# Kernel optimization log

Hardware: AMD Instinct MI355X
Metric: run time of the kernel (lower is better)

Reference implementation:

```python
import jax, jax.numpy as jnp
import numpy as np

EPS = 1e-6
NEG = 1e9

def _norm(x):
    # Normalizator math with alpha=1, gamma=0 (torch.std is unbiased -> ddof=1)
    m = jnp.mean(x, axis=-1, keepdims=True)
    s = jnp.std(x, axis=-1, ddof=1, keepdims=True)
    return (x - m) / (s + EPS)

def setup_inputs() -> dict:
    key = jax.random.key(0)
    ks = jax.random.split(key, 16)
    T, S, D, F, L = 4096, 4096, 512, 2048, 4
    sc = 1.0 / np.sqrt(D)
    scf = 1.0 / np.sqrt(F)
    return {
        "current_tgt_output": jax.random.normal(ks[0], (T, D), jnp.float32),
        "encoder_output": jax.random.normal(ks[1], (S, D), jnp.float32),
        "cross_mask": jax.random.randint(ks[2], (T, S), 0, 2).astype(jnp.float32),
        "Wq": jax.random.normal(ks[3], (L, D, D), jnp.float32) * sc,
        "Wk": jax.random.normal(ks[4], (L, D, D), jnp.float32) * sc,
        "Wv": jax.random.normal(ks[5], (L, D, D), jnp.float32) * sc,
        "Wo": jax.random.normal(ks[6], (L, D, D), jnp.float32) * sc,
        "Cq": jax.random.normal(ks[7], (L, D, D), jnp.float32) * sc,
        "Ck": jax.random.normal(ks[8], (L, D, D), jnp.float32) * sc,
        "Cv": jax.random.normal(ks[9], (L, D, D), jnp.float32) * sc,
        "Co": jax.random.normal(ks[10], (L, D, D), jnp.float32) * sc,
        "W1": jax.random.normal(ks[11], (L, D, F), jnp.float32) * sc,
        "W2": jax.random.normal(ks[12], (L, F, D), jnp.float32) * scf,
        "alpha": jnp.ones((1,), jnp.float32),
        "gamma": jnp.zeros((1,), jnp.float32),
        "input_ids": jax.random.randint(ks[13], (T,), 0, S),
        "training_step": T,
        "training_mode": 1,
    }

def reference(current_tgt_output, encoder_output, cross_mask, Wq, Wk, Wv, Wo,
              Cq, Ck, Cv, Co, W1, W2, alpha, gamma, input_ids,
              training_step, training_mode):
    T = training_step
    x = current_tgt_output[:T] if training_mode else current_tgt_output
    cm = cross_mask[:T]                                  # [T, S]
    # the python double-loop -> single vectorized gather: self_mask[i,k]=cross_mask[i, input_ids[k]]
    self_mask = cm[:, input_ids]                         # [T, T]
    sbias = (self_mask - 1.0) * NEG                      # additive mask bias
    cbias = (cm - 1.0) * NEG
    D = x.shape[-1]
    scale = 1.0 / jnp.sqrt(jnp.asarray(D, x.dtype))
    L = Wq.shape[0]
    for l in range(L):
        h = _norm(x)
        q, k, v = h @ Wq[l], h @ Wk[l], h @ Wv[l]
        a = jax.nn.softmax(q @ k.T * scale + sbias, axis=-1)
        x = x + (a @ v) @ Wo[l]
        h = _norm(x)
        q = h @ Cq[l]
        k, v = encoder_output @ Ck[l], encoder_output @ Cv[l]
        a = jax.nn.softmax(q @ k.T * scale + cbias, axis=-1)
        x = x + (a @ v) @ Co[l]
        h = _norm(x)
        x = x + jax.nn.relu(h @ W1[l]) @ W2[l]
    return alpha * _norm(x) + gamma
```

## Files before the change

### kernel.cpp

```cpp
#include <hip/hip_runtime.h>
#include <math.h>

typedef _Float16 half_t;
typedef unsigned int u32;
typedef unsigned short u16;
typedef float f32x4 __attribute__((ext_vector_type(4)));
typedef _Float16 f16x8 __attribute__((ext_vector_type(8)));
typedef _Float16 f16x4 __attribute__((ext_vector_type(4)));

#define T_DIM 4096
#define S_DIM 4096
#define D_DIM 512
#define F_DIM 2048
#define NLAYER 4
#define KVS ((size_t)4096 * 512)

__device__ __forceinline__ void gload16(const void* g, void* l) {
    __builtin_amdgcn_global_load_lds(
        (const __attribute__((address_space(1))) u32*)g,
        (__attribute__((address_space(3))) u32*)l, 16, 0, 0);
}

template<int N> __device__ __forceinline__ void wait_vm() {
    if constexpr (N == 0) asm volatile("s_waitcnt vmcnt(0)" ::: "memory");
    else if constexpr (N == 3) asm volatile("s_waitcnt vmcnt(3)" ::: "memory");
    else if constexpr (N == 4) asm volatile("s_waitcnt vmcnt(4)" ::: "memory");
    else if constexpr (N == 6) asm volatile("s_waitcnt vmcnt(6)" ::: "memory");
    else if constexpr (N == 8) asm volatile("s_waitcnt vmcnt(8)" ::: "memory");
}
__device__ __forceinline__ void wait_lgkm0() {
    asm volatile("s_waitcnt lgkmcnt(0)" ::: "memory");
}

template<int BN, int EPI>
__global__ __launch_bounds__(512)
void gemm_nt(const half_t* __restrict__ A, int lda,
             const half_t* __restrict__ B, int ldb,
             int N, int K, int gx,
             half_t* __restrict__ D1, half_t* __restrict__ D2,
             half_t* __restrict__ D3, int ldd)
{
    constexpr int BM = 128, BK = 64;
    constexpr int NF = BN / 32;
    constexpr int LPT = 2 + BN / 64;
    constexpr int NSLOT = (BN == 64) ? 3 : 2;
    __shared__ half_t As[NSLOT][BM * BK];
    __shared__ half_t Bs[NSLOT][BN * BK];

    const int tid  = threadIdx.x;
    const int wave = tid >> 6;
    const int lane = tid & 63;

    const int nb  = gridDim.x;
    const int bid = blockIdx.x;
    const int nid = (bid & 7) * (nb >> 3) + (bid >> 3);
    const int bx  = nid % gx;
    const int by  = nid / gx;
    const int bm = by * BM, bn = bx * BN;

    const int wm = (wave >> 1) * 32;
    const int wn = (wave & 1) * (BN / 2);
    const int kq = lane >> 4;
    const int rr = lane & 15;
    const int scol = (((lane & 7) ^ (lane >> 3)) << 3);

    f32x4 acc[2][NF];
#pragma unroll
    for (int m = 0; m < 2; ++m)
#pragma unroll
        for (int n = 0; n < NF; ++n)
            acc[m][n] = f32x4{0.f, 0.f, 0.f, 0.f};

    auto stage = [&](int buf, int k0) {
#pragma unroll
        for (int c = 0; c < 2; ++c) {
            const int row = wave * 16 + c * 8 + (lane >> 3);
            gload16(A + (size_t)(bm + row) * lda + k0 + scol,
                    (char*)&As[buf][0] + (wave * 2 + c) * 1024 + lane * 16);
        }
        if constexpr (BN == 64) {
            const int row = wave * 8 + (lane >> 3);
            gload16(B + (size_t)(bn + row) * ldb + k0 + scol,
                    (char*)&Bs[buf][0] + wave * 1024 + lane * 16);
        } else {
#pragma unroll
            for (int c = 0; c < 2; ++c) {
                const int row = wave * 16 + c * 8 + (lane >> 3);
                gload16(B + (size_t)(bn + row) * ldb + k0 + scol,
                        (char*)&Bs[buf][0] + (wave * 2 + c) * 1024 + lane * 16);
            }
        }
    };

    const int nt = K / BK;
    stage(0, 0);
    if constexpr (NSLOT == 3) stage(1, BK);
    int cur = 0, pf = NSLOT - 1;
    for (int t = 0; t < nt; ++t) {
        if (t + 1 < nt) wait_vm<(NSLOT - 2) * LPT>(); else wait_vm<0>();
        __builtin_amdgcn_s_barrier();
        if (t + NSLOT - 1 < nt) stage(pf, (t + NSLOT - 1) * BK);
#pragma unroll
        for (int ks = 0; ks < 2; ++ks) {
            f16x8 af[2], bf[NF];
#pragma unroll
            for (int m = 0; m < 2; ++m) {
                const int r = wm + m * 16 + rr;
                af[m] = *(const f16x8*)&As[cur][r * BK + (((ks * 4 + kq) ^ (r & 7)) << 3)];
            }
#pragma unroll
            for (int n = 0; n < NF; ++n) {
                const int r = wn + n * 16 + rr;
                bf[n] = *(const f16x8*)&Bs[cur][r * BK + (((ks * 4 + kq) ^ (r & 7)) << 3)];
            }
#pragma unroll
            for (int m = 0; m < 2; ++m)
#pragma unroll
                for (int n = 0; n < NF; ++n)
                    acc[m][n] = __builtin_amdgcn_mfma_f32_16x16x32_f16(af[m], bf[n], acc[m][n], 0, 0, 0);
        }
        cur = (cur + 1 == NSLOT) ? 0 : cur + 1;
        pf  = (pf  + 1 == NSLOT) ? 0 : pf  + 1;
    }

    const int r0 = bm + wm + (lane >> 4) * 4;
#pragma unroll
    for (int m = 0; m < 2; ++m)
#pragma unroll
        for (int n = 0; n < NF; ++n) {
            const int c = bn + wn + n * 16 + rr;
            if (EPI == 2) {
#pragma unroll
                for (int i = 0; i < 4; ++i)
                    D1[(size_t)(r0 + m * 16 + i) * ldd + c] = (half_t)acc[m][n][i];
            } else if (EPI == 5) {
                half_t* Dst = (bn < 512) ? D1 : (bn < 1024) ? D2 : D3;
                const int sub = c & 511;
#pragma unroll
                for (int i = 0; i < 4; ++i)
                    Dst[(size_t)(r0 + m * 16 + i) * 512 + sub] = (half_t)acc[m][n][i];
            } else {
                const int l = c >> 10;
                const int sub = c & 1023;
                half_t* Dst = (sub < 512) ? (D2 + l * KVS) : (D3 + l * KVS);
                const int d = sub & 511;
#pragma unroll
                for (int i = 0; i < 4; ++i)
                    Dst[(size_t)(r0 + m * 16 + i) * 512 + d] = (half_t)acc[m][n][i];
            }
        }
}

__global__ __launch_bounds__(512)
void gemm_fold(const half_t* __restrict__ Wt, const half_t* __restrict__ V,
               half_t* __restrict__ Out, int zSA, long zSB, long zSD)
{
    constexpr int BM = 128, BK = 64, BN = 64, NSLOT = 3, LPT = 3;
    __shared__ half_t As[NSLOT][BM * BK];
    __shared__ half_t Bs[NSLOT][BN * BK];

    const half_t* A = Wt + (size_t)blockIdx.z * zSA;
    const half_t* B = V  + (size_t)blockIdx.z * zSB;
    half_t* D = Out + (size_t)blockIdx.z * zSD;

    const int tid  = threadIdx.x;
    const int wave = tid >> 6;
    const int lane = tid & 63;

    const int nb  = gridDim.x;
    const int bid = blockIdx.x;
    const int nid = (bid & 7) * (nb >> 3) + (bid >> 3);
    const int bx = nid & 63, by = nid >> 6;
    const int bm = by * BM, bn = bx * BN;

    const int wm = (wave >> 1) * 32;
    const int wn = (wave & 1) * 32;
    const int kq = lane >> 4;
    const int rr = lane & 15;
    const int scol = (((lane & 7) ^ (lane >> 3)) << 3);

    f32x4 acc[2][2];
#pragma unroll
    for (int m = 0; m < 2; ++m)
#pragma unroll
        for (int n = 0; n < 2; ++n)
            acc[m][n] = f32x4{0.f, 0.f, 0.f, 0.f};

    auto stage = [&](int buf, int k0) {
#pragma unroll
        for (int c = 0; c < 2; ++c) {
            const int row = wave * 16 + c * 8 + (lane >> 3);
            gload16(A + (size_t)(bm + row) * 512 + k0 + scol,
                    (char*)&As[buf][0] + (wave * 2 + c) * 1024 + lane * 16);
        }
        const int row = wave * 8 + (lane >> 3);
        gload16(B + (size_t)(bn + row) * 512 + k0 + scol,
                (char*)&Bs[buf][0] + wave * 1024 + lane * 16);
    };

    const int nt = 512 / BK;
    stage(0, 0);
    stage(1, BK);
    int cur = 0, pf = 2;
    for (int t = 0; t < nt; ++t) {
        if (t + 1 < nt) wait_vm<LPT>(); else wait_vm<0>();
        __builtin_amdgcn_s_barrier();
        if (t + 2 < nt) stage(pf, (t + 2) * BK);
#pragma unroll
        for (int ks = 0; ks < 2; ++ks) {
            f16x8 af[2], bf[2];
#pragma unroll
            for (int m = 0; m < 2; ++m) {
                const int r = wm + m * 16 + rr;
                af[m] = *(const f16x8*)&As[cur][r * BK + (((ks * 4 + kq) ^ (r & 7)) << 3)];
            }
#pragma unroll
            for (int n = 0; n < 2; ++n) {
                const int r = wn + n * 16 + rr;
                bf[n] = *(const f16x8*)&Bs[cur][r * BK + (((ks * 4 + kq) ^ (r & 7)) << 3)];
            }
#pragma unroll
            for (int m = 0; m < 2; ++m)
#pragma unroll
                for (int n = 0; n < 2; ++n)
                    acc[m][n] = __builtin_amdgcn_mfma_f32_16x16x32_f16(af[m], bf[n], acc[m][n], 0, 0, 0);
        }
        cur = (cur + 1 == NSLOT) ? 0 : cur + 1;
        pf  = (pf  + 1 == NSLOT) ? 0 : pf  + 1;
    }

    const int r0 = bm + wm + (lane >> 4) * 4;
#pragma unroll
    for (int m = 0; m < 2; ++m)
#pragma unroll
        for (int n = 0; n < 2; ++n) {
            const int c = bn + wn + n * 16 + rr;
#pragma unroll
            for (int i = 0; i < 4; ++i)
                D[(size_t)(r0 + m * 16 + i) * 4096 + c] = (half_t)acc[m][n][i];
        }
}

template<int EPI, int SPLITK = 1, int P16 = 1>
__global__ __launch_bounds__(256)
void gemm97(const half_t* __restrict__ A, int lda,
            const half_t* __restrict__ B, int ldb,
            int K, int gx, half_t* __restrict__ D,
            float* __restrict__ Fout, int ldd)
{
    constexpr int BK = 32, NSLOT = 3, LPT = 4;
    __shared__ half_t As[NSLOT][128 * BK];
    __shared__ half_t Bs[NSLOT][128 * BK];

    const int tid  = threadIdx.x;
    const int wave = tid >> 6;
    const int lane = tid & 63;

    const int nb  = gridDim.x;
    const int bid = blockIdx.x;
    const int nid = (bid & 7) * (nb >> 3) + (bid >> 3);
    const int gy  = nb / (gx * SPLITK);
    const int bx  = nid % gx;
    const int tmp = nid / gx;
    const int by  = tmp % gy;
    const int kz  = tmp / gy;
    const int bm = by * 128, bn = bx * 128;

    const int Keff = K / SPLITK;
    A += (size_t)kz * Keff;
    B += (size_t)kz * Keff;

    const int wm = (wave >> 1) * 64;
    const int wn = (wave & 1) * 64;
    const int kq = lane >> 4;
    const int rr = lane & 15;
    const int srow = lane >> 2;
    const int scol = (((lane & 3) ^ ((lane >> 3) & 3)) << 3);
    const int kqa  = kq ^ ((rr >> 1) & 3);

    const half_t* Abase = A + (size_t)(bm + wave * 16 + srow) * lda + scol;
    const half_t* Bbase = B + (size_t)(bn + wave * 16 + srow) * ldb + scol;

    f32x4 acc[4][4];
#pragma unroll
    for (int m = 0; m < 4; ++m)
#pragma unroll
        for (int n = 0; n < 4; ++n)
            acc[m][n] = f32x4{0.f, 0.f, 0.f, 0.f};

    auto stage = [&](int buf, int k0) {
#pragma unroll
        for (int c = 0; c < 2; ++c)
            gload16(Abase + (size_t)c * 64 * lda + k0,
                    (char*)&As[buf][0] + c * 4096 + wave * 1024 + lane * 16);
#pragma unroll
        for (int c = 0; c < 2; ++c)
            gload16(Bbase + (size_t)c * 64 * ldb + k0,
                    (char*)&Bs[buf][0] + c * 4096 + wave * 1024 + lane * 16);
    };

    const int nt = Keff / BK;
    stage(0, 0);
    stage(1, BK);
    int cur = 0, pf = 2;
    for (int t = 0; t < nt; ++t) {
        if (t + 1 < nt) wait_vm<LPT>(); else wait_vm<0>();
        __builtin_amdgcn_s_barrier();
        if (t + 2 < nt) stage(pf, (t + 2) * BK);
        f16x8 af[4], bf[4];
#pragma unroll
        for (int m = 0; m < 4; ++m)
            af[m] = *(const f16x8*)&As[cur][(wm + m * 16 + rr) * BK + kqa * 8];
#pragma unroll
        for (int n = 0; n < 4; ++n)
            bf[n] = *(const f16x8*)&Bs[cur][(wn + n * 16 + rr) * BK + kqa * 8];
#pragma unroll
        for (int m = 0; m < 4; ++m)
#pragma unroll
            for (int n = 0; n < 4; ++n)
                acc[m][n] = __builtin_amdgcn_mfma_f32_16x16x32_f16(af[m], bf[n], acc[m][n], 0, 0, 0);
        cur = (cur == 2) ? 0 : cur + 1;
        pf  = (pf  == 2) ? 0 : pf + 1;
    }

    const int r0 = bm + wm + (lane >> 4) * 4;
    const int soff = kz * gx * 128;
#pragma unroll
    for (int m = 0; m < 4; ++m)
#pragma unroll
        for (int n = 0; n < 4; ++n) {
            const int c = bn + wn + n * 16 + rr;
#pragma unroll
            for (int i = 0; i < 4; ++i) {
                float v = acc[m][n][i];
                const size_t r = r0 + m * 16 + i;
                if constexpr (SPLITK > 1) {
                    if constexpr (P16) D[r * ldd + soff + c] = (half_t)v;
                    else               Fout[r * ldd + soff + c] = v;
                } else {
                    if (EPI == 4) v = fmaxf(v, 0.f);
                    D[r * ldd + c] = (half_t)v;
                }
            }
        }
}

__global__ __launch_bounds__(256, 4)
void gemm_logits(const half_t* __restrict__ A, const half_t* __restrict__ B,
                 const u32* __restrict__ bits, half_t* __restrict__ D)
{
    constexpr int BK = 32, NSLOT = 3, LPT = 4, nt = 16;
    __shared__ half_t As[NSLOT][128 * BK];
    __shared__ half_t Bs[NSLOT][128 * BK];

    const int tid  = threadIdx.x;
    const int wave = tid >> 6;
    const int lane = tid & 63;

    const int nb  = gridDim.x;
    const int bid = blockIdx.x;
    const int nid = (bid & 7) * (nb >> 3) + (bid >> 3);
    const int bx = nid & 31, by = nid >> 5;
    const int bm = by * 128, bn = bx * 128;

    const int wm = (wave >> 1) * 64;
    const int wn = (wave & 1) * 64;
    const int kq = lane >> 4;
    const int rr = lane & 15;
    const int srow = lane >> 2;
    const int scol = (((lane & 3) ^ ((lane >> 3) & 3)) << 3);
    const int kqa  = kq ^ ((rr >> 1) & 3);

    const half_t* Abase = A + (size_t)(bm + wave * 16 + srow) * 512 + scol;
    const half_t* Bbase = B + (size_t)(bn + wave * 16 + srow) * 512 + scol;

    f32x4 acc[4][4];
#pragma unroll
    for (int m = 0; m < 4; ++m)
#pragma unroll
        for (int n = 0; n < 4; ++n)
            acc[m][n] = f32x4{0.f, 0.f, 0.f, 0.f};

    auto stage = [&](int buf, int k0) {
#pragma unroll
        for (int c = 0; c < 2; ++c)
            gload16(Abase + (size_t)c * 64 * 512 + k0,
                    (char*)&As[buf][0] + c * 4096 + wave * 1024 + lane * 16);
#pragma unroll
        for (int c = 0; c < 2; ++c)
            gload16(Bbase + (size_t)c * 64 * 512 + k0,
                    (char*)&Bs[buf][0] + c * 4096 + wave * 1024 + lane * 16);
    };

    stage(0, 0);
    stage(1, BK);
    int cur = 0, pf = 2;
    for (int t = 0; t < nt; ++t) {
        if (t + 1 < nt) wait_vm<LPT>(); else wait_vm<0>();
        __builtin_amdgcn_s_barrier();
        if (t + 2 < nt) stage(pf, (t + 2) * BK);
        f16x8 af[4], bf[4];
#pragma unroll
        for (int m = 0; m < 4; ++m)
            af[m] = *(const f16x8*)&As[cur][(wm + m * 16 + rr) * BK + kqa * 8];
#pragma unroll
        for (int n = 0; n < 4; ++n)
            bf[n] = *(const f16x8*)&Bs[cur][(wn + n * 16 + rr) * BK + kqa * 8];
#pragma unroll
        for (int m = 0; m < 4; ++m)
#pragma unroll
            for (int n = 0; n < 4; ++n)
                acc[m][n] = __builtin_amdgcn_mfma_f32_16x16x32_f16(af[m], bf[n], acc[m][n], 0, 0, 0);
        cur = (cur == 2) ? 0 : cur + 1;
        pf  = (pf  == 2) ? 0 : pf + 1;
    }

    const int g4 = (lane >> 4) * 4;
    const int r0 = bm + wm + g4;
    const int wordbase = (bn + wn) >> 5;
#pragma unroll
    for (int m = 0; m < 4; ++m)
#pragma unroll
        for (int i = 0; i < 4; ++i) {
            const int r = r0 + m * 16 + i;
            const u32 w01 = bits[(size_t)r * 128 + wordbase];
            const u32 w23 = bits[(size_t)r * 128 + wordbase + 1];
            acc[m][0][i] += (((w01 >> rr) & 1u) ? 0.f : -1e9f);
            acc[m][1][i] += (((w01 >> (16 + rr)) & 1u) ? 0.f : -1e9f);
            acc[m][2][i] += (((w23 >> rr) & 1u) ? 0.f : -1e9f);
            acc[m][3][i] += (((w23 >> (16 + rr)) & 1u) ? 0.f : -1e9f);
        }
#pragma unroll
    for (int m = 0; m < 4; ++m)
#pragma unroll
        for (int n = 0; n < 4; ++n) {
            const int c = bn + wn + n * 16 + rr;
#pragma unroll
            for (int i = 0; i < 4; ++i)
                D[(size_t)(r0 + m * 16 + i) * 4096 + c] = (half_t)acc[m][n][i];
        }
}

__global__ __launch_bounds__(256)
void row_stats(const half_t* __restrict__ logits, float2* __restrict__ rowstat)
{
    const int t = blockIdx.x;
    const half_t* row = logits + (size_t)t * S_DIM;
    __shared__ float red[8];
    const int tid = threadIdx.x, wave = tid >> 6, lane = tid & 63;
    const int s0 = tid * 16;
    f16x8 h0 = *(const f16x8*)&row[s0];
    f16x8 h1 = *(const f16x8*)&row[s0 + 8];
    float z[16];
    float lmax = -3.0e38f;
#pragma unroll
    for (int q = 0; q < 16; ++q) {
        z[q] = (float)((q < 8) ? h0[q & 7] : h1[q & 7]);
        lmax = fmaxf(lmax, z[q]);
    }
#pragma unroll
    for (int off = 32; off; off >>= 1) lmax = fmaxf(lmax, __shfl_xor(lmax, off));
    if (lane == 0) red[wave] = lmax;
    __syncthreads();
    const float mx = fmaxf(fmaxf(red[0], red[1]), fmaxf(red[2], red[3]));
    float lsum = 0.f;
#pragma unroll
    for (int q = 0; q < 16; ++q) lsum += __expf(z[q] - mx);
#pragma unroll
    for (int off = 32; off; off >>= 1) lsum += __shfl_xor(lsum, off);
    if (lane == 0) red[4 + wave] = lsum;
    __syncthreads();
    if (tid == 0)
        rowstat[t] = float2{mx, 1.f / (red[4] + red[5] + red[6] + red[7])};
}

__global__ __launch_bounds__(256)
void gemm_pv(const half_t* __restrict__ A, const half_t* __restrict__ B,
             const float2* __restrict__ rowstat, half_t* __restrict__ D)
{
    constexpr int BK = 32, NSLOT = 3, Keff = 1024, nt = 32;
    __shared__ half_t As[NSLOT][128 * BK];
    __shared__ half_t Bs[NSLOT][128 * BK];

    const int tid = threadIdx.x, wave = tid >> 6, lane = tid & 63;
    const int nb = gridDim.x, bid = blockIdx.x;
    const int nid = (bid & 7) * (nb >> 3) + (bid >> 3);
    const int bx = nid & 3;
    const int tmp = nid >> 2;
    const int by = tmp & 31, kz = tmp >> 5;
    const int bm = by * 128, bn = bx * 128;

    const int wm = (wave >> 1) * 64, wn = (wave & 1) * 64;
    const int kq = lane >> 4, rr = lane & 15, srow = lane >> 2;
    const int scol = (((lane & 3) ^ ((lane >> 3) & 3)) << 3);
    const int kqa = kq ^ ((rr >> 1) & 3);

    const int arow = bm + wave * 16 + srow;
    const half_t* Abase = A + (size_t)arow * 4096 + kz * Keff + scol;
    const half_t* Bbase = B + (size_t)(bn + wave * 16 + srow) * 4096 + kz * Keff + scol;

    const float2 rs0 = rowstat[arow];
    const float2 rs1 = rowstat[arow + 64];
    asm volatile("s_waitcnt vmcnt(0)" ::: "memory");
    const float M0 = rs0.x, I0 = rs0.y, M1 = rs1.x, I1 = rs1.y;

    f32x4 acc[4][4];
#pragma unroll
    for (int m = 0; m < 4; ++m)
#pragma unroll
        for (int n = 0; n < 4; ++n)
            acc[m][n] = f32x4{0.f, 0.f, 0.f, 0.f};

    auto loadA = [&](int k0, f16x8& a0, f16x8& a1) {
        a0 = *(const f16x8*)(Abase + k0);
        a1 = *(const f16x8*)(Abase + (size_t)64 * 4096 + k0);
    };
    auto gloadB = [&](int buf, int k0) {
        gload16(Bbase + k0, (char*)&Bs[buf][0] + wave * 1024 + lane * 16);
        gload16(Bbase + (size_t)64 * 4096 + k0,
                (char*)&Bs[buf][0] + 4096 + wave * 1024 + lane * 16);
    };
    auto writeA = [&](int buf, const f16x8& a0, const f16x8& a1) {
        f16x8 p0, p1;
#pragma unroll
        for (int e = 0; e < 8; ++e) {
            p0[e] = (half_t)(__expf((float)a0[e] - M0) * I0);
            p1[e] = (half_t)(__expf((float)a1[e] - M1) * I1);
        }
        *(f16x8*)((char*)&As[buf][0] + wave * 1024 + lane * 16) = p0;
        *(f16x8*)((char*)&As[buf][0] + 4096 + wave * 1024 + lane * 16) = p1;
    };
    auto compute = [&](int s) {
        f16x8 af[4], bf[4];
#pragma unroll
        for (int m = 0; m < 4; ++m)
            af[m] = *(const f16x8*)&As[s][(wm + m * 16 + rr) * BK + kqa * 8];
#pragma unroll
        for (int n = 0; n < 4; ++n)
            bf[n] = *(const f16x8*)&Bs[s][(wn + n * 16 + rr) * BK + kqa * 8];
#pragma unroll
        for (int m = 0; m < 4; ++m)
#pragma unroll
            for (int n = 0; n < 4; ++n)
                acc[m][n] = __builtin_amdgcn_mfma_f32_16x16x32_f16(af[m], bf[n], acc[m][n], 0, 0, 0);
    };

    f16x8 a0A, a1A, a0B, a1B;
    loadA(0, a0A, a1A);  gloadB(0, 0);
    loadA(BK, a0B, a1B); gloadB(1, BK);
    wait_vm<4>();
    writeA(0, a0A, a1A);
    wait_lgkm0();
    __builtin_amdgcn_s_barrier();

    int cur = 0, pf = 2;
    for (int t = 0; t < nt; t += 2) {
        {
            const bool hasPF = (t + 2 < nt);
            if (hasPF) { loadA((t + 2) * BK, a0A, a1A); gloadB(pf, (t + 2) * BK); }
            compute(cur);
            if (t + 1 < nt) {
                if (hasPF) wait_vm<4>(); else wait_vm<0>();
                writeA((cur + 1 == NSLOT) ? 0 : cur + 1, a0B, a1B);
                wait_lgkm0();
            }
            __builtin_amdgcn_s_barrier();
            cur = (cur + 1 == NSLOT) ? 0 : cur + 1;
            pf  = (pf  + 1 == NSLOT) ? 0 : pf + 1;
        }
        {
            const int u = t + 1;
            const bool hasPF = (u + 2 < nt);
            if (hasPF) { loadA((u + 2) * BK, a0B, a1B); gloadB(pf, (u + 2) * BK); }
            compute(cur);
            if (u + 1 < nt) {
                if (hasPF) wait_vm<4>(); else wait_vm<0>();
                writeA((cur + 1 == NSLOT) ? 0 : cur + 1, a0A, a1A);
                wait_lgkm0();
            }
            __builtin_amdgcn_s_barrier();
            cur = (cur + 1 == NSLOT) ? 0 : cur + 1;
            pf  = (pf  + 1 == NSLOT) ? 0 : pf + 1;
        }
    }

    const int r0 = bm + wm + (lane >> 4) * 4;
    const int soff = kz * 512;
#pragma unroll
    for (int m = 0; m < 4; ++m)
#pragma unroll
        for (int n = 0; n < 4; ++n) {
            const int c = bn + wn + n * 16 + rr;
#pragma unroll
            for (int i = 0; i < 4; ++i)
                D[(size_t)(r0 + m * 16 + i) * 2048 + soff + c] = (half_t)acc[m][n][i];
        }
}

__global__ __launch_bounds__(256)
void attn_tail(const float* __restrict__ xin, const half_t* __restrict__ P,
               float* __restrict__ xbuf, half_t* __restrict__ hh)
{
    const int row  = blockIdx.x * 4 + (threadIdx.x >> 6);
    const int lane = threadIdx.x & 63;
    const int d0 = lane * 8;
    float v[8];
    {
        const float* xr = xin + (size_t)row * D_DIM + d0;
        float4 a = *(const float4*)xr;
        float4 b = *(const float4*)(xr + 4);
        v[0]=a.x; v[1]=a.y; v[2]=a.z; v[3]=a.w; v[4]=b.x; v[5]=b.y; v[6]=b.z; v[7]=b.w;
    }
    const half_t* pr = P + (size_t)row * 2048 + d0;
#pragma unroll
    for (int j = 0; j < 4; ++j) {
        f16x8 pv = *(const f16x8*)(pr + j * 512);
#pragma unroll
        for (int e = 0; e < 8; ++e) v[e] += (float)pv[e];
    }
    float* xo = xbuf + (size_t)row * D_DIM + d0;
    *(float4*)xo       = float4{v[0], v[1], v[2], v[3]};
    *(float4*)(xo + 4) = float4{v[4], v[5], v[6], v[7]};

    float s = 0.f;
#pragma unroll
    for (int j = 0; j < 8; ++j) s += v[j];
#pragma unroll
    for (int off = 32; off; off >>= 1) s += __shfl_xor(s, off);
    const float mean = s * (1.f / 512.f);
    float ss = 0.f;
#pragma unroll
    for (int j = 0; j < 8; ++j) { float d = v[j] - mean; ss += d * d; }
#pragma unroll
    for (int off = 32; off; off >>= 1) ss += __shfl_xor(ss, off);
    const float inv = 1.f / (sqrtf(ss * (1.f / 511.f)) + 1e-6f);
    f16x8 hv;
#pragma unroll
    for (int j = 0; j < 8; ++j) hv[j] = (half_t)((v[j] - mean) * inv);
    *(f16x8*)&hh[(size_t)row * D_DIM + d0] = hv;
}

template<int FINAL>
__global__ __launch_bounds__(256)
void norm_red(const float* __restrict__ xin, const float* __restrict__ P,
              float* __restrict__ xbuf, half_t* __restrict__ hh,
              float* __restrict__ outF, const float* __restrict__ alphaP,
              const float* __restrict__ gammaP)
{
    const int row  = blockIdx.x * 4 + (threadIdx.x >> 6);
    const int lane = threadIdx.x & 63;
    const int d0 = lane * 8;
    const float* xr = xin + (size_t)row * D_DIM + d0;
    float v[8];
    {
        float4 a = *(const float4*)xr;
        float4 b = *(const float4*)(xr + 4);
        v[0]=a.x; v[1]=a.y; v[2]=a.z; v[3]=a.w; v[4]=b.x; v[5]=b.y; v[6]=b.z; v[7]=b.w;
    }
    const float* pr = P + (size_t)row * 2048 + d0;
#pragma unroll
    for (int j = 0; j < 4; ++j) {
        float4 a = *(const float4*)(pr + j * 512);
        float4 b = *(const float4*)(pr + j * 512 + 4);
        v[0]+=a.x; v[1]+=a.y; v[2]+=a.z; v[3]+=a.w; v[4]+=b.x; v[5]+=b.y; v[6]+=b.z; v[7]+=b.w;
    }
    if (!FINAL) {
        float* xo = xbuf + (size_t)row * D_DIM + d0;
        *(float4*)xo       = float4{v[0], v[1], v[2], v[3]};
        *(float4*)(xo + 4) = float4{v[4], v[5], v[6], v[7]};
    }
    float s = 0.f;
#pragma unroll
    for (int j = 0; j < 8; ++j) s += v[j];
#pragma unroll
    for (int off = 32; off; off >>= 1) s += __shfl_xor(s, off);
    const float mean = s * (1.f / 512.f);
    float ss = 0.f;
#pragma unroll
    for (int j = 0; j < 8; ++j) { float d = v[j] - mean; ss += d * d; }
#pragma unroll
    for (int off = 32; off; off >>= 1) ss += __shfl_xor(ss, off);
    const float inv = 1.f / (sqrtf(ss * (1.f / 511.f)) + 1e-6f);
    if (FINAL) {
        const float alp = alphaP[0], gam = gammaP[0];
        float o[8];
#pragma unroll
        for (int j = 0; j < 8; ++j) o[j] = alp * ((v[j] - mean) * inv) + gam;
        float* op = outF + (size_t)row * D_DIM + d0;
        *(float4*)op       = float4{o[0], o[1], o[2], o[3]};
        *(float4*)(op + 4) = float4{o[4], o[5], o[6], o[7]};
    } else {
        f16x8 hv;
#pragma unroll
        for (int j = 0; j < 8; ++j) hv[j] = (half_t)((v[j] - mean) * inv);
        *(f16x8*)&hh[(size_t)row * D_DIM + d0] = hv;
    }
}

template<int FINAL>
__global__ __launch_bounds__(256)
void norm_rows(const float* __restrict__ x, half_t* __restrict__ hh,
               float* __restrict__ outF, const float* __restrict__ alphaP,
               const float* __restrict__ gammaP)
{
    const int row  = blockIdx.x * 4 + (threadIdx.x >> 6);
    const int lane = threadIdx.x & 63;
    const float* xr = x + (size_t)row * D_DIM + lane * 8;
    float4 a = *(const float4*)xr;
    float4 b = *(const float4*)(xr + 4);
    float v[8] = {a.x, a.y, a.z, a.w, b.x, b.y, b.z, b.w};
    float s = 0.f;
#pragma unroll
    for (int j = 0; j < 8; ++j) s += v[j];
#pragma unroll
    for (int off = 32; off; off >>= 1) s += __shfl_xor(s, off);
    const float mean = s * (1.f / 512.f);
    float ss = 0.f;
#pragma unroll
    for (int j = 0; j < 8; ++j) { float d = v[j] - mean; ss += d * d; }
#pragma unroll
    for (int off = 32; off; off >>= 1) ss += __shfl_xor(ss, off);
    const float inv = 1.f / (sqrtf(ss * (1.f / 511.f)) + 1e-6f);
    if (FINAL) {
        const float alp = alphaP[0], gam = gammaP[0];
        float o[8];
#pragma unroll
        for (int j = 0; j < 8; ++j) o[j] = alp * ((v[j] - mean) * inv) + gam;
        float* op = outF + (size_t)row * D_DIM + lane * 8;
        *(float4*)op       = float4{o[0], o[1], o[2], o[3]};
        *(float4*)(op + 4) = float4{o[4], o[5], o[6], o[7]};
    } else {
        f16x8 hv;
#pragma unroll
        for (int j = 0; j < 8; ++j) hv[j] = (half_t)((v[j] - mean) * inv);
        *(f16x8*)&hh[(size_t)row * D_DIM + lane * 8] = hv;
    }
}

__global__ __launch_bounds__(256)
void cast_f16(const float* __restrict__ in, half_t* __restrict__ out)
{
    size_t i = ((size_t)blockIdx.x * 256 + threadIdx.x) * 8;
    float4 a = *(const float4*)&in[i];
    float4 b = *(const float4*)&in[i + 4];
    float v[8] = {a.x, a.y, a.z, a.w, b.x, b.y, b.z, b.w};
    f16x8 o;
#pragma unroll
    for (int j = 0; j < 8; ++j) o[j] = (half_t)v[j];
    *(f16x8*)&out[i] = o;
}

__global__ __launch_bounds__(256)
void transpose_cast8(const float* __restrict__ i0, const float* __restrict__ i1,
                     const float* __restrict__ i2, const float* __restrict__ i3,
                     const float* __restrict__ i4, const float* __restrict__ i5,
                     const float* __restrict__ i6, const float* __restrict__ i7,
                     half_t* __restrict__ o0, half_t* __restrict__ o1,
                     half_t* __restrict__ o2, half_t* __restrict__ o3,
                     half_t* __restrict__ o4, half_t* __restrict__ o5,
                     half_t* __restrict__ o6, half_t* __restrict__ o7,
                     float qscale)
{
    const int SQ = 512 * 512, QKVZ = 1536 * 512, KVZ = 1024 * 512;
    const int z = blockIdx.z, t = z >> 2, l = z & 3;
    const float* in; half_t* out; float sc = 1.f; int outZ;
    switch (t) {
        case 0: in = i0; out = o0; sc = qscale; outZ = QKVZ; break;
        case 1: in = i1; out = o1; outZ = QKVZ; break;
        case 2: in = i2; out = o2; outZ = QKVZ; break;
        case 3: in = i3; out = o3; outZ = SQ; break;
        case 4: in = i4; out = o4; sc = qscale; outZ = SQ; break;
        case 5: in = i5; out = o5; outZ = KVZ; break;
        case 6: in = i6; out = o6; outZ = KVZ; break;
        default: in = i7; out = o7; outZ = SQ; break;
    }
    in  += (size_t)l * SQ;
    out += (size_t)l * outZ;
    __shared__ float tile[32][33];
    const int tx = threadIdx.x & 31, ty = threadIdx.x >> 5;
    const int r0 = blockIdx.y * 32, c0 = blockIdx.x * 32;
#pragma unroll
    for (int i = 0; i < 4; ++i)
        tile[ty + i * 8][tx] = in[(size_t)(r0 + ty + i * 8) * 512 + c0 + tx];
    __syncthreads();
#pragma unroll
    for (int i = 0; i < 4; ++i)
        out[(size_t)(c0 + ty + i * 8) * 512 + r0 + tx] = (half_t)(tile[tx][ty + i * 8] * sc);
}

__global__ __launch_bounds__(256)
void transpose_cast(const float* __restrict__ in, half_t* __restrict__ out,
                    int R, int C, float scale, int inZ, int outZ)
{
    in  += (size_t)blockIdx.z * inZ;
    out += (size_t)blockIdx.z * outZ;
    __shared__ float tile[32][33];
    const int tx = threadIdx.x & 31, ty = threadIdx.x >> 5;
    const int r0 = blockIdx.y * 32, c0 = blockIdx.x * 32;
#pragma unroll
    for (int i = 0; i < 4; ++i)
        tile[ty + i * 8][tx] = in[(size_t)(r0 + ty + i * 8) * C + c0 + tx];
    __syncthreads();
#pragma unroll
    for (int i = 0; i < 4; ++i)
        out[(size_t)(c0 + ty + i * 8) * R + r0 + tx] = (half_t)(tile[tx][ty + i * 8] * scale);
}

__global__ __launch_bounds__(256)
void pack_masks(const float* __restrict__ cm, const int* __restrict__ ids,
                u32* __restrict__ crossb, u32* __restrict__ selfb)
{
    const int t = blockIdx.x;
    const float* row = cm + (size_t)t * S_DIM;
    __shared__ u32 cb[S_DIM / 32];
    __shared__ u16 sh16[256];
    const int tid = threadIdx.x;
    u32 bits = 0;
#pragma unroll
    for (int q = 0; q < 4; ++q) {
        float4 v = *(const float4*)&row[tid * 16 + q * 4];
        bits |= (v.x > 0.5f ? 1u : 0u) << (q * 4 + 0);
        bits |= (v.y > 0.5f ? 1u : 0u) << (q * 4 + 1);
        bits |= (v.z > 0.5f ? 1u : 0u) << (q * 4 + 2);
        bits |= (v.w > 0.5f ? 1u : 0u) << (q * 4 + 3);
    }
    ((u16*)cb)[tid] = (u16)bits;
    __syncthreads();
    u32 sb = 0;
#pragma unroll
    for (int q = 0; q < 4; ++q) {
        int4 id4 = *(const int4*)&ids[tid * 16 + q * 4];
        sb |= ((cb[id4.x >> 5] >> (id4.x & 31)) & 1u) << (q * 4 + 0);
        sb |= ((cb[id4.y >> 5] >> (id4.y & 31)) & 1u) << (q * 4 + 1);
        sb |= ((cb[id4.z >> 5] >> (id4.z & 31)) & 1u) << (q * 4 + 2);
        sb |= ((cb[id4.w >> 5] >> (id4.w & 31)) & 1u) << (q * 4 + 3);
    }
    sh16[tid] = (u16)sb;
    __syncthreads();
    if (tid < 128) {
        crossb[(size_t)t * 128 + tid] = cb[tid];
        selfb[(size_t)t * 128 + tid]  = (u32)sh16[2 * tid] | ((u32)sh16[2 * tid + 1] << 16);
    }
}

extern "C" void kernel_launch(void* const* d_in, const int* in_sizes, int n_in,
                              void* d_out, int out_size, void* d_ws, size_t ws_size,
                              hipStream_t stream)
{
    (void)in_sizes; (void)n_in; (void)out_size; (void)ws_size;

    const float* x0p  = (const float*)d_in[0];
    const float* encp = (const float*)d_in[1];
    const float* cmp  = (const float*)d_in[2];
    const float* Wq = (const float*)d_in[3], *Wk = (const float*)d_in[4];
    const float* Wv = (const float*)d_in[5], *Wo = (const float*)d_in[6];
    const float* Cq = (const float*)d_in[7], *Ck = (const float*)d_in[8];
    const float* Cv = (const float*)d_in[9], *Co = (const float*)d_in[10];
    const float* W1p = (const float*)d_in[11];
    const float* W2p = (const float*)d_in[12];
    const float* alphap = (const float*)d_in[13];
    const float* gammap = (const float*)d_in[14];
    const int*   idsp   = (const int*)d_in[15];
    float* outp = (float*)d_out;

    char* wp = (char*)d_ws;
    auto take = [&](size_t nelem, int esz) -> void* {
        void* p = (void*)wp;
        wp += (nelem * (size_t)esz + 255) & ~(size_t)255;
        return p;
    };
    half_t* wqkvT = (half_t*)take((size_t)NLAYER * 1536 * 512, 2);
    half_t* ckvT  = (half_t*)take((size_t)NLAYER * 1024 * 512, 2);
    half_t* cqT   = (half_t*)take((size_t)NLAYER * 512 * 512, 2);
    half_t* woT   = (half_t*)take((size_t)NLAYER * 512 * 512, 2);
    half_t* coT   = (half_t*)take((size_t)NLAYER * 512 * 512, 2);
    half_t* w1T   = (half_t*)take((size_t)NLAYER * D_DIM * F_DIM, 2);
    half_t* w2T   = (half_t*)take((size_t)NLAYER * D_DIM * F_DIM, 2);
    half_t* hh    = (half_t*)take((size_t)T_DIM * D_DIM, 2);
    half_t* qb    = (half_t*)take((size_t)T_DIM * D_DIM, 2);
    half_t* kb    = (half_t*)take((size_t)S_DIM * D_DIM, 2);
    half_t* vb    = (half_t*)take((size_t)S_DIM * D_DIM, 2);
    half_t* vTp   = (half_t*)take((size_t)S_DIM * D_DIM, 2);
    half_t* mid   = (half_t*)take((size_t)T_DIM * F_DIM, 2);
    half_t* enc16 = (half_t*)take((size_t)S_DIM * D_DIM, 2);
    half_t* kbC   = (half_t*)take((size_t)NLAYER * S_DIM * D_DIM, 2);
    half_t* vC    = (half_t*)take((size_t)NLAYER * S_DIM * D_DIM, 2);
    half_t* vTCp  = (half_t*)take((size_t)NLAYER * S_DIM * D_DIM, 2);
    float* xbuf   = (float*)take((size_t)T_DIM * D_DIM, 4);
    half_t* logit16 = (half_t*)take((size_t)T_DIM * S_DIM, 2);
    half_t* p16   = (half_t*)take((size_t)T_DIM * 2048, 2);
    float* pbuf   = (float*)take((size_t)T_DIM * 2048, 4);
    float2* rowstat = (float2*)take((size_t)T_DIM, 8);
    u32* crossb = (u32*)take((size_t)T_DIM * (S_DIM / 32), 4);
    u32* selfb  = (u32*)take((size_t)T_DIM * (S_DIM / 32), 4);

    const dim3 B(256), B512(512);
    const float qscale = 0.04419417382415922f;

    const int SQ = 512 * 512, FZ = 512 * 2048;
    transpose_cast8<<<dim3(16, 16, 32), B, 0, stream>>>(
        Wq, Wk, Wv, Wo, Cq, Ck, Cv, Co,
        wqkvT, wqkvT + SQ, wqkvT + 2 * SQ, woT, cqT, ckvT, ckvT + SQ, coT, qscale);
    transpose_cast<<<dim3(64,16,4), B, 0, stream>>>(W1p, w1T, 512, 2048, 1.f, FZ, FZ);
    transpose_cast<<<dim3(16,64,4), B, 0, stream>>>(W2p, w2T, 2048, 512, 1.f, FZ, FZ);
    cast_f16<<<dim3((S_DIM * D_DIM / 8) / 256), B, 0, stream>>>(encp, enc16);
    pack_masks<<<dim3(T_DIM), B, 0, stream>>>(cmp, idsp, crossb, selfb);
    gemm_nt<64, 7><<<dim3(2048), B512, 0, stream>>>(enc16, 512, ckvT, 512,
        4096, 512, 64, nullptr, kbC, vC, 0);
    gemm_fold<<<dim3(256, 1, NLAYER), B512, 0, stream>>>(coT, vC, vTCp,
        SQ, (long)KVS, (long)KVS);

    for (int l = 0; l < NLAYER; ++l) {
        if (l == 0)
            norm_rows<0><<<T_DIM / 4, B, 0, stream>>>(x0p, hh, nullptr, nullptr, nullptr);
        else
            norm_red<0><<<T_DIM / 4, B, 0, stream>>>(xbuf, pbuf, xbuf, hh, nullptr, nullptr, nullptr);

        gemm_nt<64, 5><<<dim3(768), B512, 0, stream>>>(hh, 512, wqkvT + (size_t)l * 1536 * 512, 512,
            1536, 512, 24, qb, kb, vb, 0);
        gemm_fold<<<dim3(256, 1, 1), B512, 0, stream>>>(woT + (size_t)l * SQ, vb, vTp, 0, 0, 0);
        gemm_logits<<<dim3(1024), B, 0, stream>>>(qb, kb, selfb, logit16);
        row_stats<<<dim3(T_DIM), B, 0, stream>>>(logit16, rowstat);
        gemm_pv<<<dim3(512), B, 0, stream>>>(logit16, vTp, rowstat, p16);
        attn_tail<<<dim3(T_DIM / 4), B, 0, stream>>>((l == 0) ? x0p : xbuf, p16, xbuf, hh);

        gemm_nt<64, 2><<<dim3(256), B512, 0, stream>>>(hh, 512, cqT + (size_t)l * SQ, 512,
            512, 512, 8, qb, nullptr, nullptr, 512);
        gemm_logits<<<dim3(1024), B, 0, stream>>>(qb, kbC + (size_t)l * KVS, crossb, logit16);
        row_stats<<<dim3(T_DIM), B, 0, stream>>>(logit16, rowstat);
        gemm_pv<<<dim3(512), B, 0, stream>>>(logit16, vTCp + (size_t)l * KVS, rowstat, p16);
        attn_tail<<<dim3(T_DIM / 4), B, 0, stream>>>(xbuf, p16, xbuf, hh);

        gemm97<4><<<dim3(512), B, 0, stream>>>(hh, 512, w1T + (size_t)l * FZ, 512,
            512, 16, mid, nullptr, 2048);
        gemm97<0, 4, 0><<<dim3(512), B, 0, stream>>>(mid, 2048, w2T + (size_t)l * FZ, 2048,
            2048, 4, nullptr, pbuf, 2048);
    }

    norm_red<1><<<T_DIM / 4, B, 0, stream>>>(xbuf, pbuf, xbuf, nullptr, outp, alphap, gammap);
}
```

Before: 1.218 ms.

## Drop dedicated masked-logits GEMM; apply bit mask in row_stats and PV

Removes the specialized gemm_logits kernel and computes raw QK^T logits with the generic gemm97 kernel instead. The attention mask bits are now applied later: row_stats masks values before the max and sum reductions, and gemm_pv zeroes masked probabilities while building P, loading the mask words alongside its A tiles. This removes the mask epilogue from the logits GEMM, but each mask word is now read twice, once in row_stats and once in gemm_pv. gemm_pv carries extra per-element selects and a deeper vmcnt wait. Correctness depends on gemm97<2> with these arguments producing the intended 4096x4096 fp16 logits.

Result: no change. 1.195 ms (-1.9%).

```diff
diff --git a/kernel.cpp b/kernel.cpp
--- a/kernel.cpp
+++ b/kernel.cpp
@@ -345,117 +345,25 @@
         }
 }
 
-__global__ __launch_bounds__(256, 4)
-void gemm_logits(const half_t* __restrict__ A, const half_t* __restrict__ B,
-                 const u32* __restrict__ bits, half_t* __restrict__ D)
-{
-    constexpr int BK = 32, NSLOT = 3, LPT = 4, nt = 16;
-    __shared__ half_t As[NSLOT][128 * BK];
-    __shared__ half_t Bs[NSLOT][128 * BK];
-
-    const int tid  = threadIdx.x;
-    const int wave = tid >> 6;
-    const int lane = tid & 63;
-
-    const int nb  = gridDim.x;
-    const int bid = blockIdx.x;
-    const int nid = (bid & 7) * (nb >> 3) + (bid >> 3);
-    const int bx = nid & 31, by = nid >> 5;
-    const int bm = by * 128, bn = bx * 128;
-
-    const int wm = (wave >> 1) * 64;
-    const int wn = (wave & 1) * 64;
-    const int kq = lane >> 4;
-    const int rr = lane & 15;
-    const int srow = lane >> 2;
-    const int scol = (((lane & 3) ^ ((lane >> 3) & 3)) << 3);
-    const int kqa  = kq ^ ((rr >> 1) & 3);
-
-    const half_t* Abase = A + (size_t)(bm + wave * 16 + srow) * 512 + scol;
-    const half_t* Bbase = B + (size_t)(bn + wave * 16 + srow) * 512 + scol;
-
-    f32x4 acc[4][4];
-#pragma unroll
-    for (int m = 0; m < 4; ++m)
-#pragma unroll
-        for (int n = 0; n < 4; ++n)
-            acc[m][n] = f32x4{0.f, 0.f, 0.f, 0.f};
-
-    auto stage = [&](int buf, int k0) {
-#pragma unroll
-        for (int c = 0; c < 2; ++c)
-            gload16(Abase + (size_t)c * 64 * 512 + k0,
-                    (char*)&As[buf][0] + c * 4096 + wave * 1024 + lane * 16);
-#pragma unroll
-        for (int c = 0; c < 2; ++c)
-            gload16(Bbase + (size_t)c * 64 * 512 + k0,
-                    (char*)&Bs[buf][0] + c * 4096 + wave * 1024 + lane * 16);
-    };
-
-    stage(0, 0);
-    stage(1, BK);
-    int cur = 0, pf = 2;
-    for (int t = 0; t < nt; ++t) {
-        if (t + 1 < nt) wait_vm<LPT>(); else wait_vm<0>();
-        __builtin_amdgcn_s_barrier();
-        if (t + 2 < nt) stage(pf, (t + 2) * BK);
-        f16x8 af[4], bf[4];
-#pragma unroll
-        for (int m = 0; m < 4; ++m)
-            af[m] = *(const f16x8*)&As[cur][(wm + m * 16 + rr) * BK + kqa * 8];
-#pragma unroll
-        for (int n = 0; n < 4; ++n)
-            bf[n] = *(const f16x8*)&Bs[cur][(wn + n * 16 + rr) * BK + kqa * 8];
-#pragma unroll
-        for (int m = 0; m < 4; ++m)
-#pragma unroll
-            for (int n = 0; n < 4; ++n)
-                acc[m][n] = __builtin_amdgcn_mfma_f32_16x16x32_f16(af[m], bf[n], acc[m][n], 0, 0, 0);
-        cur = (cur == 2) ? 0 : cur + 1;
-        pf  = (pf  == 2) ? 0 : pf + 1;
-    }
-
-    const int g4 = (lane >> 4) * 4;
-    const int r0 = bm + wm + g4;
-    const int wordbase = (bn + wn) >> 5;
-#pragma unroll
-    for (int m = 0; m < 4; ++m)
-#pragma unroll
-        for (int i = 0; i < 4; ++i) {
-            const int r = r0 + m * 16 + i;
-            const u32 w01 = bits[(size_t)r * 128 + wordbase];
-            const u32 w23 = bits[(size_t)r * 128 + wordbase + 1];
-            acc[m][0][i] += (((w01 >> rr) & 1u) ? 0.f : -1e9f);
-            acc[m][1][i] += (((w01 >> (16 + rr)) & 1u) ? 0.f : -1e9f);
-            acc[m][2][i] += (((w23 >> rr) & 1u) ? 0.f : -1e9f);
-            acc[m][3][i] += (((w23 >> (16 + rr)) & 1u) ? 0.f : -1e9f);
-        }
-#pragma unroll
-    for (int m = 0; m < 4; ++m)
-#pragma unroll
-        for (int n = 0; n < 4; ++n) {
-            const int c = bn + wn + n * 16 + rr;
-#pragma unroll
-            for (int i = 0; i < 4; ++i)
-                D[(size_t)(r0 + m * 16 + i) * 4096 + c] = (half_t)acc[m][n][i];
-        }
-}
-
-__global__ __launch_bounds__(256)
-void row_stats(const half_t* __restrict__ logits, float2* __restrict__ rowstat)
+__global__ __launch_bounds__(256)
+void row_stats(const half_t* __restrict__ logits, const u32* __restrict__ bits,
+               float2* __restrict__ rowstat)
 {
     const int t = blockIdx.x;
     const half_t* row = logits + (size_t)t * S_DIM;
+    const u32* bw = bits + (size_t)t * (S_DIM / 32);
     __shared__ float red[8];
     const int tid = threadIdx.x, wave = tid >> 6, lane = tid & 63;
     const int s0 = tid * 16;
     f16x8 h0 = *(const f16x8*)&row[s0];
     f16x8 h1 = *(const f16x8*)&row[s0 + 8];
+    const u32 w = bw[tid >> 1] >> ((tid & 1) * 16);
     float z[16];
     float lmax = -3.0e38f;
 #pragma unroll
     for (int q = 0; q < 16; ++q) {
-        z[q] = (float)((q < 8) ? h0[q & 7] : h1[q & 7]);
+        const float v = (float)((q < 8) ? h0[q & 7] : h1[q & 7]);
+        z[q] = ((w >> q) & 1u) ? v : -1e9f;
         lmax = fmaxf(lmax, z[q]);
     }
 #pragma unroll
@@ -465,7 +373,8 @@
     const float mx = fmaxf(fmaxf(red[0], red[1]), fmaxf(red[2], red[3]));
     float lsum = 0.f;
 #pragma unroll
-    for (int q = 0; q < 16; ++q) lsum += __expf(z[q] - mx);
+    for (int q = 0; q < 16; ++q)
+        lsum += (z[q] > -1e8f) ? __expf(z[q] - mx) : 0.f;
 #pragma unroll
     for (int off = 32; off; off >>= 1) lsum += __shfl_xor(lsum, off);
     if (lane == 0) red[4 + wave] = lsum;
@@ -476,7 +385,8 @@
 
 __global__ __launch_bounds__(256)
 void gemm_pv(const half_t* __restrict__ A, const half_t* __restrict__ B,
-             const float2* __restrict__ rowstat, half_t* __restrict__ D)
+             const u32* __restrict__ bits, const float2* __restrict__ rowstat,
+             half_t* __restrict__ D)
 {
     constexpr int BK = 32, NSLOT = 3, Keff = 1024, nt = 32;
     __shared__ half_t As[NSLOT][128 * BK];
@@ -498,6 +408,8 @@
     const int arow = bm + wave * 16 + srow;
     const half_t* Abase = A + (size_t)arow * 4096 + kz * Keff + scol;
     const half_t* Bbase = B + (size_t)(bn + wave * 16 + srow) * 4096 + kz * Keff + scol;
+    const u32* Wbase0 = bits + (size_t)arow * 128 + (kz * Keff >> 5);
+    const u32* Wbase1 = bits + (size_t)(arow + 64) * 128 + (kz * Keff >> 5);
 
     const float2 rs0 = rowstat[arow];
     const float2 rs1 = rowstat[arow + 64];
@@ -511,21 +423,25 @@
         for (int n = 0; n < 4; ++n)
             acc[m][n] = f32x4{0.f, 0.f, 0.f, 0.f};
 
-    auto loadA = [&](int k0, f16x8& a0, f16x8& a1) {
+    auto loadA = [&](int k0, f16x8& a0, f16x8& a1, u32& w0, u32& w1) {
         a0 = *(const f16x8*)(Abase + k0);
         a1 = *(const f16x8*)(Abase + (size_t)64 * 4096 + k0);
+        w0 = Wbase0[k0 >> 5];
+        w1 = Wbase1[k0 >> 5];
     };
     auto gloadB = [&](int buf, int k0) {
         gload16(Bbase + k0, (char*)&Bs[buf][0] + wave * 1024 + lane * 16);
         gload16(Bbase + (size_t)64 * 4096 + k0,
                 (char*)&Bs[buf][0] + 4096 + wave * 1024 + lane * 16);
     };
-    auto writeA = [&](int buf, const f16x8& a0, const f16x8& a1) {
+    auto writeA = [&](int buf, const f16x8& a0, const f16x8& a1, u32 w0, u32 w1) {
         f16x8 p0, p1;
 #pragma unroll
         for (int e = 0; e < 8; ++e) {
-            p0[e] = (half_t)(__expf((float)a0[e] - M0) * I0);
-            p1[e] = (half_t)(__expf((float)a1[e] - M1) * I1);
+            const float e0 = __expf((float)a0[e] - M0) * I0;
+            const float e1 = __expf((float)a1[e] - M1) * I1;
+            p0[e] = (half_t)(((w0 >> (scol + e)) & 1u) ? e0 : 0.f);
+            p1[e] = (half_t)(((w1 >> (scol + e)) & 1u) ? e1 : 0.f);
         }
         *(f16x8*)((char*)&As[buf][0] + wave * 1024 + lane * 16) = p0;
         *(f16x8*)((char*)&As[buf][0] + 4096 + wave * 1024 + lane * 16) = p1;
@@ -546,10 +462,11 @@
     };
 
     f16x8 a0A, a1A, a0B, a1B;
-    loadA(0, a0A, a1A);  gloadB(0, 0);
-    loadA(BK, a0B, a1B); gloadB(1, BK);
-    wait_vm<4>();
-    writeA(0, a0A, a1A);
+    u32 w0A, w1A, w0B, w1B;
+    loadA(0, a0A, a1A, w0A, w1A);  gloadB(0, 0);
+    loadA(BK, a0B, a1B, w0B, w1B); gloadB(1, BK);
+    wait_vm<6>();
+    writeA(0, a0A, a1A, w0A, w1A);
     wait_lgkm0();
     __builtin_amdgcn_s_barrier();
 
@@ -557,11 +474,11 @@
     for (int t = 0; t < nt; t += 2) {
         {
             const bool hasPF = (t + 2 < nt);
-            if (hasPF) { loadA((t + 2) * BK, a0A, a1A); gloadB(pf, (t + 2) * BK); }
+            if (hasPF) { loadA((t + 2) * BK, a0A, a1A, w0A, w1A); gloadB(pf, (t + 2) * BK); }
             compute(cur);
             if (t + 1 < nt) {
-                if (hasPF) wait_vm<4>(); else wait_vm<0>();
-                writeA((cur + 1 == NSLOT) ? 0 : cur + 1, a0B, a1B);
+                if (hasPF) wait_vm<6>(); else wait_vm<0>();
+                writeA((cur + 1 == NSLOT) ? 0 : cur + 1, a0B, a1B, w0B, w1B);
                 wait_lgkm0();
             }
             __builtin_amdgcn_s_barrier();
@@ -571,11 +488,11 @@
         {
             const int u = t + 1;
             const bool hasPF = (u + 2 < nt);
-            if (hasPF) { loadA((u + 2) * BK, a0B, a1B); gloadB(pf, (u + 2) * BK); }
+            if (hasPF) { loadA((u + 2) * BK, a0B, a1B, w0B, w1B); gloadB(pf, (u + 2) * BK); }
             compute(cur);
             if (u + 1 < nt) {
-                if (hasPF) wait_vm<4>(); else wait_vm<0>();
-                writeA((cur + 1 == NSLOT) ? 0 : cur + 1, a0A, a1A);
+                if (hasPF) wait_vm<6>(); else wait_vm<0>();
+                writeA((cur + 1 == NSLOT) ? 0 : cur + 1, a0A, a1A, w0A, w1A);
                 wait_lgkm0();
             }
             __builtin_amdgcn_s_barrier();
@@ -919,16 +836,18 @@
         gemm_nt<64, 5><<<dim3(768), B512, 0, stream>>>(hh, 512, wqkvT + (size_t)l * 1536 * 512, 512,
             1536, 512, 24, qb, kb, vb, 0);
         gemm_fold<<<dim3(256, 1, 1), B512, 0, stream>>>(woT + (size_t)l * SQ, vb, vTp, 0, 0, 0);
-        gemm_logits<<<dim3(1024), B, 0, stream>>>(qb, kb, selfb, logit16);
-        row_stats<<<dim3(T_DIM), B, 0, stream>>>(logit16, rowstat);
-        gemm_pv<<<dim3(512), B, 0, stream>>>(logit16, vTp, rowstat, p16);
+        gemm97<2><<<dim3(1024), B, 0, stream>>>(qb, 512, kb, 512,
+            512, 32, logit16, nullptr, 4096);
+        row_stats<<<dim3(T_DIM), B, 0, stream>>>(logit16, selfb, rowstat);
+        gemm_pv<<<dim3(512), B, 0, stream>>>(logit16, vTp, selfb, rowstat, p16);
         attn_tail<<<dim3(T_DIM / 4), B, 0, stream>>>((l == 0) ? x0p : xbuf, p16, xbuf, hh);
 
         gemm_nt<64, 2><<<dim3(256), B512, 0, stream>>>(hh, 512, cqT + (size_t)l * SQ, 512,
             512, 512, 8, qb, nullptr, nullptr, 512);
-        gemm_logits<<<dim3(1024), B, 0, stream>>>(qb, kbC + (size_t)l * KVS, crossb, logit16);
-        row_stats<<<dim3(T_DIM), B, 0, stream>>>(logit16, rowstat);
-        gemm_pv<<<dim3(512), B, 0, stream>>>(logit16, vTCp + (size_t)l * KVS, rowstat, p16);
+        gemm97<2><<<dim3(1024), B, 0, stream>>>(qb, 512, kbC + (size_t)l * KVS, 512,
+            512, 32, logit16, nullptr, 4096);
+        row_stats<<<dim3(T_DIM), B, 0, stream>>>(logit16, crossb, rowstat);
+        gemm_pv<<<dim3(512), B, 0, stream>>>(logit16, vTCp + (size_t)l * KVS, crossb, rowstat, p16);
         attn_tail<<<dim3(T_DIM / 4), B, 0, stream>>>(xbuf, p16, xbuf, hh);
 
         gemm97<4><<<dim3(512), B, 0, stream>>>(hh, 512, w1T + (size_t)l * FZ, 512,
```
